# Performance work log

Hardware: AMD Instinct MI355X
Metric: run time of the kernel (lower is better)

## Reference

```python
import jax, jax.numpy as jnp
import numpy as np

N, C, H, W = 16, 512, 32, 32
NH = 8            # num_heads
HD = C // NH      # head dim c = 64
G = C // 4        # GroupNorm groups = 128
EPS = 1e-5


def conv1x1(X, Wt, b):
    # 1x1 Conv2d == per-pixel linear over channels
    return jnp.einsum('oc,nchw->nohw', Wt, X) + b[None, :, None, None]


def setup_inputs() -> dict:
    key = jax.random.key(0)
    ks = jax.random.split(key, 9)
    s = 0.02
    inp = {
        'X': jax.random.normal(ks[0], (N, C, H, W), jnp.float32),
        'Wq': jax.random.normal(ks[1], (C, C), jnp.float32) * s,
        'bq': jax.random.normal(ks[2], (C,), jnp.float32) * s,
        'Wk': jax.random.normal(ks[3], (C, C), jnp.float32) * s,
        'bk': jax.random.normal(ks[4], (C,), jnp.float32) * s,
        'Wv': jax.random.normal(ks[5], (C, C), jnp.float32) * s,
        'bv': jax.random.normal(ks[6], (C,), jnp.float32) * s,
        'Wo': jax.random.normal(ks[7], (C, C), jnp.float32) * s,
        'bo': jax.random.normal(ks[8], (C,), jnp.float32) * s,
        'gn_w': jnp.ones((C,), jnp.float32),
        'gn_b': jnp.zeros((C,), jnp.float32),
    }
    return inp


def reference(X, Wq, bq, Wk, bk, Wv, bv, Wo, bo, gn_w, gn_b):
    # NOTE: original torch code does  K, Q, V = (Q_conv(X), K_conv(X), V_conv(X))
    # i.e. K gets the Q_conv weights and Q gets the K_conv weights; mirror that.
    K = conv1x1(X, Wq, bq)
    Q = conv1x1(X, Wk, bk)
    V = conv1x1(X, Wv, bv)

    d = H * W
    Kh = K.reshape(N, NH, HD, d)  # [n,h,c,d]
    Qh = Q.reshape(N, NH, HD, d)
    Vh = V.reshape(N, NH, HD, d)

    # softmax-free channel attention: (Q^T K) then V (Q^T K)^T
    A = jnp.einsum('nhcd,nhcD->nhdD', Qh, Kh)   # [n,h,d,d]
    O = jnp.einsum('nhdD,nhcD->nhcd', A, Vh)    # [n,h,c,d]

    O = O.reshape(N, C, H, W)
    O = conv1x1(O, Wo, bo)

    # GroupNorm(G, C) with affine, eps=1e-5
    Og = O.reshape(N, G, C // G, H, W)
    mu = Og.mean(axis=(2, 3, 4), keepdims=True)
    var = Og.var(axis=(2, 3, 4), keepdims=True)
    On = ((Og - mu) * jax.lax.rsqrt(var + EPS)).reshape(N, C, H, W)
    On = On * gn_w[None, :, None, None] + gn_b[None, :, None, None]

    return On + X
```

## Files before the change

kernel.cpp:

```cpp
#include <hip/hip_runtime.h>
#include <hip/hip_bf16.h>

typedef __attribute__((ext_vector_type(8))) short s8v;
typedef __attribute__((ext_vector_type(4))) short s4v;
typedef __attribute__((ext_vector_type(4))) float f32x4;

#define MFMA_BF16 __builtin_amdgcn_mfma_f32_16x16x32_bf16

__device__ inline void gload_lds16(const __hip_bfloat16* g, __hip_bfloat16* l) {
  __builtin_amdgcn_global_load_lds(
      (const __attribute__((address_space(1))) void*)g,
      (__attribute__((address_space(3))) void*)l, 16, 0, 0);
}

__device__ inline short f2bs(float x) {
  __hip_bfloat16 b = __float2bfloat16(x);
  return *reinterpret_cast<short*>(&b);
}

__device__ inline void storeC(float* p, float v) { *p = v; }
__device__ inline void storeC(__hip_bfloat16* p, float v) { *p = __float2bfloat16(v); }

__global__ __launch_bounds__(256) void prep(const float* __restrict__ X,
                                            __hip_bfloat16* __restrict__ XT,
                                            __hip_bfloat16* __restrict__ Xc,
                                            const float* __restrict__ Wq,
                                            const float* __restrict__ Wv,
                                            const float* __restrict__ Wk,
                                            const float* __restrict__ Wo,
                                            const float* __restrict__ bq,
                                            const float* __restrict__ bv,
                                            __hip_bfloat16* __restrict__ WA,
                                            __hip_bfloat16* __restrict__ WkT,
                                            __hip_bfloat16* __restrict__ WOb,
                                            float* __restrict__ biasKV) {
  const int tid = threadIdx.x;
  if (blockIdx.z == 16) {
    const int blk = blockIdx.y * 16 + blockIdx.x;
#pragma unroll
    for (int t = 0; t < 8; ++t) {
      const int i = (blk * 8 + t) * 256 + tid;
      WA[i] = __float2bfloat16(Wq[i]);
      WA[262144 + i] = __float2bfloat16(Wv[i]);
      WOb[i] = __float2bfloat16(Wo[i]);
      WkT[i] = __float2bfloat16(Wk[(i & 511) * 512 + (i >> 9)]);
      if (i < 512) { biasKV[i] = bq[i]; biasKV[512 + i] = bv[i]; }
    }
    return;
  }
  __shared__ float tl[64][65];
  const int n = blockIdx.z;
  const int c0 = blockIdx.y * 64, p0 = blockIdx.x * 64;
  const int lr = tid >> 4, lc4 = (tid & 15) * 4;
  const float* Xp = X + ((long)n * 512 + c0) * 1024 + p0;
  __hip_bfloat16* Xcp = Xc + ((long)n * 512 + c0) * 1024 + p0;
#pragma unroll
  for (int i = 0; i < 4; ++i) {
    const int ch = i * 16 + lr;
    const float4 v = *(const float4*)&Xp[(long)ch * 1024 + lc4];
    tl[ch][lc4 + 0] = v.x; tl[ch][lc4 + 1] = v.y;
    tl[ch][lc4 + 2] = v.z; tl[ch][lc4 + 3] = v.w;
    s4v xo;
    xo[0] = f2bs(v.x); xo[1] = f2bs(v.y); xo[2] = f2bs(v.z); xo[3] = f2bs(v.w);
    *(s4v*)&Xcp[(long)ch * 1024 + lc4] = xo;
  }
  __syncthreads();
  __hip_bfloat16* XTp = XT + ((long)n * 1024 + p0) * 512 + c0;
#pragma unroll
  for (int i = 0; i < 4; ++i) {
    const int px = i * 16 + lr;
    s4v o;
#pragma unroll
    for (int e = 0; e < 4; ++e) o[e] = f2bs(tl[lc4 + e][px]);
    *(s4v*)&XTp[(long)px * 512 + lc4] = o;
  }
}

template <typename OutT, bool BROW>
__global__ __launch_bounds__(256) void gemm_nt(
    const __hip_bfloat16* __restrict__ A, long strideA,
    const __hip_bfloat16* __restrict__ B, long strideB,
    OutT* __restrict__ C, long strideC, int K, int ldc,
    const float* __restrict__ brow, long strideBrow) {
  A += blockIdx.z * strideA;
  B += blockIdx.z * strideB;
  C += blockIdx.z * strideC;
  const int m0 = blockIdx.y * 128;
  const int n0 = blockIdx.x * 128;
  const int tid = threadIdx.x;
  const int wid = tid >> 6, lane = tid & 63;
  const int wm = wid >> 1, wn = wid & 1;

  __shared__ __hip_bfloat16 As[128 * 64];
  __shared__ __hip_bfloat16 Bs[128 * 64];

  f32x4 acc[4][4] = {};

  const __hip_bfloat16* gA0 = A + (long)(m0 + wid * 32 + (lane >> 3)) * K + (lane & 7) * 8;
  const __hip_bfloat16* gB0 = B + (long)(n0 + wid * 32 + (lane >> 3)) * K + (lane & 7) * 8;

  for (int k0 = 0; k0 < K; k0 += 64) {
#pragma unroll
    for (int t = 0; t < 4; ++t) {
      gload_lds16(gA0 + (long)t * 8 * K + k0, &As[(wid * 32 + t * 8) * 64]);
      gload_lds16(gB0 + (long)t * 8 * K + k0, &Bs[(wid * 32 + t * 8) * 64]);
    }
    __syncthreads();
#pragma unroll
    for (int ks = 0; ks < 2; ++ks) {
      const int koff = ks * 32 + (lane >> 4) * 8;
      s8v a[4], b[4];
#pragma unroll
      for (int i = 0; i < 4; ++i)
        a[i] = *(const s8v*)&As[(wm * 64 + i * 16 + (lane & 15)) * 64 + koff];
#pragma unroll
      for (int j = 0; j < 4; ++j)
        b[j] = *(const s8v*)&Bs[(wn * 64 + j * 16 + (lane & 15)) * 64 + koff];
#pragma unroll
      for (int i = 0; i < 4; ++i)
#pragma unroll
        for (int j = 0; j < 4; ++j)
          acc[i][j] = MFMA_BF16(a[i], b[j], acc[i][j], 0, 0, 0);
    }
    __syncthreads();
  }

  const int cr = (lane >> 4) * 4;
  const int cc = lane & 15;
#pragma unroll
  for (int i = 0; i < 4; ++i) {
#pragma unroll
    for (int r = 0; r < 4; ++r) {
      const int gm = m0 + wm * 64 + i * 16 + cr + r;
      const float rb = BROW ? brow[blockIdx.z * strideBrow + gm] : 0.f;
#pragma unroll
      for (int j = 0; j < 4; ++j) {
        const int gn = n0 + wn * 64 + j * 16 + cc;
        storeC(&C[(long)gm * ldc + gn], acc[i][j][r] + rb);
      }
    }
  }
}

__global__ __launch_bounds__(512) void gemm_vkT(const __hip_bfloat16* __restrict__ V,
                                                const __hip_bfloat16* __restrict__ Kk,
                                                __hip_bfloat16* __restrict__ Mt) {
  const int n = blockIdx.x >> 3, h = blockIdx.x & 7;
  const int tid = threadIdx.x, wid = tid >> 6, lane = tid & 63;
  f32x4 acc[4][4] = {};
  const long colbase = (long)n * 1024 + wid * 128 + (lane >> 4) * 8;
  const __hip_bfloat16* Vb = V + (long)(h * 64 + (lane & 15)) * 16384 + colbase;
  const __hip_bfloat16* Kb = Kk + (long)(h * 64 + (lane & 15)) * 16384 + colbase;
#pragma unroll
  for (int kk = 0; kk < 128; kk += 32) {
    s8v a[4], b[4];
#pragma unroll
    for (int i = 0; i < 4; ++i) a[i] = *(const s8v*)(Vb + (long)i * 16 * 16384 + kk);
#pragma unroll
    for (int j = 0; j < 4; ++j) b[j] = *(const s8v*)(Kb + (long)j * 16 * 16384 + kk);
#pragma unroll
    for (int i = 0; i < 4; ++i)
#pragma unroll
      for (int j = 0; j < 4; ++j) acc[i][j] = MFMA_BF16(a[i], b[j], acc[i][j], 0, 0, 0);
  }
  __shared__ float part[4][4096];
  const int cr = (lane >> 4) * 4, cc = lane & 15;
  if (wid < 4) {
#pragma unroll
    for (int i = 0; i < 4; ++i)
#pragma unroll
      for (int r = 0; r < 4; ++r)
#pragma unroll
        for (int j = 0; j < 4; ++j)
          part[wid][(i * 16 + cr + r) * 64 + j * 16 + cc] = acc[i][j][r];
  }
  __syncthreads();
  if (wid >= 4) {
#pragma unroll
    for (int i = 0; i < 4; ++i)
#pragma unroll
      for (int r = 0; r < 4; ++r)
#pragma unroll
        for (int j = 0; j < 4; ++j)
          part[wid - 4][(i * 16 + cr + r) * 64 + j * 16 + cc] += acc[i][j][r];
  }
  __syncthreads();
  __hip_bfloat16* outp = Mt + ((long)n * 8 + h) * 4096;
  for (int e = tid; e < 4096; e += 512) {
    const float sum = part[0][e] + part[1][e] + part[2][e] + part[3][e];
    outp[(e & 63) * 64 + (e >> 6)] = __float2bfloat16(sum);
  }
}

__global__ __launch_bounds__(256) void wchain(const __hip_bfloat16* __restrict__ WOb,
                                              const __hip_bfloat16* __restrict__ WkT,
                                              const __hip_bfloat16* __restrict__ Mt,
                                              const float* __restrict__ bk,
                                              const float* __restrict__ bo,
                                              __hip_bfloat16* __restrict__ WPP,
                                              float* __restrict__ b2out) {
  const int c0 = blockIdx.x * 128, o0 = blockIdx.y * 128, n = blockIdx.z;
  const int tid = threadIdx.x, wid = tid >> 6, lane = tid & 63;
  const int wm = wid >> 1, wn = wid & 1;
  const int cr = (lane >> 4) * 4, cc = lane & 15;

  __shared__ __hip_bfloat16 WoS[128 * 64];
  __shared__ __hip_bfloat16 WkS[128 * 64];
  __shared__ __hip_bfloat16 MtS[64 * 64];
  __shared__ __hip_bfloat16 W1S[128 * 64];
  __shared__ float bkS[512];

  if (tid < 128) *(float4*)&bkS[tid * 4] = *(const float4*)&bk[tid * 4];

  f32x4 acc2[4][4] = {};
  float bacc = 0.f;
  const int r8 = lane >> 3, b8 = (lane & 7) * 8;

  for (int h = 0; h < 8; ++h) {
#pragma unroll
    for (int t = 0; t < 4; ++t) {
      const int row = wid * 32 + t * 8;
      gload_lds16(WOb + (long)(o0 + row + r8) * 512 + h * 64 + b8, &WoS[row * 64]);
      gload_lds16(WkT + (long)(c0 + row + r8) * 512 + h * 64 + b8, &WkS[row * 64]);
    }
    {
      const __hip_bfloat16* mg = Mt + ((long)n * 8 + h) * 4096;
      gload_lds16(mg + wid * 512 + lane * 8, &MtS[wid * 512]);
      gload_lds16(mg + 2048 + wid * 512 + lane * 8, &MtS[2048 + wid * 512]);
    }
    __syncthreads();

    f32x4 acc1[2][4] = {};
#pragma unroll
    for (int ks = 0; ks < 2; ++ks) {
      const int ko = ks * 32 + (lane >> 4) * 8;
      s8v aj[2], bw[4];
#pragma unroll
      for (int i = 0; i < 2; ++i)
        aj[i] = *(const s8v*)&MtS[(wn * 32 + i * 16 + cc) * 64 + ko];
#pragma unroll
      for (int t = 0; t < 4; ++t)
        bw[t] = *(const s8v*)&WoS[(wm * 64 + t * 16 + cc) * 64 + ko];
#pragma unroll
      for (int i = 0; i < 2; ++i)
#pragma unroll
        for (int t = 0; t < 4; ++t)
          acc1[i][t] = MFMA_BF16(aj[i], bw[t], acc1[i][t], 0, 0, 0);
    }
#pragma unroll
    for (int i = 0; i < 2; ++i)
#pragma unroll
      for (int t = 0; t < 4; ++t) {
        const int o = wm * 64 + t * 16 + cc;
        const int jb = wn * 32 + i * 16 + cr;
        s4v p;
#pragma unroll
        for (int r = 0; r < 4; ++r) p[r] = f2bs(acc1[i][t][r]);
        *(s4v*)((char*)W1S + ((o * 128 + jb * 2) ^ ((o & 7) << 4))) = p;
      }
    __syncthreads();

#pragma unroll
    for (int ks = 0; ks < 2; ++ks) {
      const int ko = ks * 32 + (lane >> 4) * 8;
      s8v a2[4], bw[4];
#pragma unroll
      for (int i = 0; i < 4; ++i) {
        const int o = wm * 64 + i * 16 + cc;
        a2[i] = *(const s8v*)((char*)W1S + ((o * 128 + ko * 2) ^ ((o & 7) << 4)));
      }
#pragma unroll
      for (int t = 0; t < 4; ++t)
        bw[t] = *(const s8v*)&WkS[(wn * 64 + t * 16 + cc) * 64 + ko];
#pragma unroll
      for (int i = 0; i < 4; ++i)
#pragma unroll
        for (int t = 0; t < 4; ++t)
          acc2[i][t] = MFMA_BF16(a2[i], bw[t], acc2[i][t], 0, 0, 0);
    }

    if (c0 == 0) {
      const int o = tid >> 1, half = tid & 1;
      float s = 0.f;
#pragma unroll
      for (int q = 0; q < 4; ++q) {
        const int jb = half * 64 + q * 16;
        const s8v w = *(const s8v*)((char*)W1S + ((o * 128 + jb) ^ ((o & 7) << 4)));
        const __hip_bfloat16* wb = (const __hip_bfloat16*)&w;
#pragma unroll
        for (int e = 0; e < 8; ++e)
          s += __bfloat162float(wb[e]) * bkS[h * 64 + half * 32 + q * 8 + e];
      }
      bacc += s;
    }
    __syncthreads();
  }

#pragma unroll
  for (int i = 0; i < 4; ++i)
#pragma unroll
    for (int r = 0; r < 4; ++r)
#pragma unroll
      for (int t = 0; t < 4; ++t)
        WPP[((long)n * 512 + o0 + wm * 64 + i * 16 + cr + r) * 512 +
            c0 + wn * 64 + t * 16 + cc] = __float2bfloat16(acc2[i][t][r]);
  if (c0 == 0) {
    const float tot = bacc + __shfl_xor(bacc, 1);
    if ((tid & 1) == 0) {
      const int o = tid >> 1;
      b2out[n * 512 + o0 + o] = tot + bo[o0 + o];
    }
  }
}

__global__ __launch_bounds__(256) void gn_res(const __hip_bfloat16* __restrict__ Y,
                                              const __hip_bfloat16* __restrict__ Xc,
                                              const float* __restrict__ gw,
                                              const float* __restrict__ gb,
                                              float* __restrict__ out) {
  const int n = blockIdx.x >> 7, g = blockIdx.x & 127;
  const long base = ((long)n * 512 + g * 4) * 1024;
  const int tid = threadIdx.x;
  float v[16];
  float s = 0.f, s2 = 0.f;
#pragma unroll
  for (int i = 0; i < 2; ++i) {
    const s8v x = *(const s8v*)&Y[base + ((long)(i * 256 + tid)) * 8];
#pragma unroll
    for (int e = 0; e < 8; ++e) {
      const float f = __bfloat162float(((const __hip_bfloat16*)&x)[e]);
      v[i * 8 + e] = f;
      s += f;
      s2 += f * f;
    }
  }
#pragma unroll
  for (int off = 32; off; off >>= 1) {
    s += __shfl_down(s, off);
    s2 += __shfl_down(s2, off);
  }
  __shared__ float rs[8];
  const int wid = tid >> 6, lane = tid & 63;
  if (lane == 0) { rs[wid] = s; rs[4 + wid] = s2; }
  __syncthreads();
  if (tid == 0) {
    const float ts = rs[0] + rs[1] + rs[2] + rs[3];
    const float t2 = rs[4] + rs[5] + rs[6] + rs[7];
    const float mu = ts * (1.f / 4096.f);
    const float var = t2 * (1.f / 4096.f) - mu * mu;
    rs[0] = mu;
    rs[1] = rsqrtf(var + 1e-5f);
  }
  __syncthreads();
  const float mu = rs[0], rstd = rs[1];
#pragma unroll
  for (int i = 0; i < 2; ++i) {
    const int chunk = i * 256 + tid;
    const long e0 = base + (long)chunk * 8;
    const int c = g * 4 + (chunk >> 7);
    const float sc = rstd * gw[c], sh = gb[c];
    const s8v xv = *(const s8v*)&Xc[e0];
    const __hip_bfloat16* xb = (const __hip_bfloat16*)&xv;
    float4 o0, o1;
    o0.x = (v[i * 8 + 0] - mu) * sc + sh + __bfloat162float(xb[0]);
    o0.y = (v[i * 8 + 1] - mu) * sc + sh + __bfloat162float(xb[1]);
    o0.z = (v[i * 8 + 2] - mu) * sc + sh + __bfloat162float(xb[2]);
    o0.w = (v[i * 8 + 3] - mu) * sc + sh + __bfloat162float(xb[3]);
    o1.x = (v[i * 8 + 4] - mu) * sc + sh + __bfloat162float(xb[4]);
    o1.y = (v[i * 8 + 5] - mu) * sc + sh + __bfloat162float(xb[5]);
    o1.z = (v[i * 8 + 6] - mu) * sc + sh + __bfloat162float(xb[6]);
    o1.w = (v[i * 8 + 7] - mu) * sc + sh + __bfloat162float(xb[7]);
    *(float4*)&out[e0] = o0;
    *(float4*)&out[e0 + 4] = o1;
  }
}

extern "C" void kernel_launch(void* const* d_in, const int* in_sizes, int n_in,
                              void* d_out, int out_size, void* d_ws, size_t ws_size,
                              hipStream_t stream) {
  const float* X  = (const float*)d_in[0];
  const float* Wq = (const float*)d_in[1];
  const float* bq = (const float*)d_in[2];
  const float* Wk = (const float*)d_in[3];
  const float* bk = (const float*)d_in[4];
  const float* Wv = (const float*)d_in[5];
  const float* bv = (const float*)d_in[6];
  const float* Wo = (const float*)d_in[7];
  const float* bo = (const float*)d_in[8];
  const float* gw = (const float*)d_in[9];
  const float* gb = (const float*)d_in[10];
  float* out = (float*)d_out;

  char* ws = (char*)d_ws;
  __hip_bfloat16* XT  = (__hip_bfloat16*)(ws + 0);
  __hip_bfloat16* KV  = (__hip_bfloat16*)(ws + 16777216);
  __hip_bfloat16* Y   = (__hip_bfloat16*)(ws + 16777216);
  __hip_bfloat16* WPP = (__hip_bfloat16*)(ws + 58720256);
  __hip_bfloat16* Mt  = (__hip_bfloat16*)(ws + 67108864);
  __hip_bfloat16* WA  = (__hip_bfloat16*)(ws + 68157440);
  __hip_bfloat16* WkT = (__hip_bfloat16*)(ws + 69206016);
  __hip_bfloat16* WOb = (__hip_bfloat16*)(ws + 69730304);
  float*          bKV = (float*)(ws + 70254592);
  float*          b2  = (float*)(ws + 70258688);
  __hip_bfloat16* Xc  = (__hip_bfloat16*)(ws + 75497472);

  prep<<<dim3(16, 8, 17), 256, 0, stream>>>(X, XT, Xc, Wq, Wv, Wk, Wo, bq, bv,
                                            WA, WkT, WOb, bKV);
  gemm_nt<__hip_bfloat16, true><<<dim3(128, 8, 1), 256, 0, stream>>>(
      WA, 0, XT, 0, KV, 0, 512, 16384, bKV, 0);
  gemm_vkT<<<128, 512, 0, stream>>>(KV + (long)512 * 16384, KV, Mt);
  wchain<<<dim3(4, 4, 16), 256, 0, stream>>>(WOb, WkT, Mt, bk, bo, WPP, b2);
  gemm_nt<__hip_bfloat16, true><<<dim3(8, 4, 16), 256, 0, stream>>>(
      WPP, 262144, XT, 524288, Y, 524288, 512, 1024, b2, 512);
  gn_res<<<2048, 256, 0, stream>>>(Y, Xc, gw, gb, out);
}
```

Baseline: 117.1 us.

## Double-buffer wchain LDS tiles to prefetch the next head during compute

Doubles the Wo, Wk and Mt shared-memory tiles in the wchain kernel so the loads for head h+1 are issued while head h is being computed. The plain __syncthreads calls are replaced with explicit waitcnt plus s_barrier pairs, and the barrier at the end of each iteration is dropped. The aim is to hide global-to-LDS load latency behind the two MFMA stages. In exchange, LDS use per block grows substantially, which can lower occupancy, and correctness now depends on the hand-placed waits.

```diff
diff --git a/kernel.cpp b/kernel.cpp
--- a/kernel.cpp
+++ b/kernel.cpp
@@ -204,31 +204,38 @@
   const int wm = wid >> 1, wn = wid & 1;
   const int cr = (lane >> 4) * 4, cc = lane & 15;
 
-  __shared__ __hip_bfloat16 WoS[128 * 64];
-  __shared__ __hip_bfloat16 WkS[128 * 64];
-  __shared__ __hip_bfloat16 MtS[64 * 64];
+  __shared__ __hip_bfloat16 WoS[2][128 * 64];
+  __shared__ __hip_bfloat16 WkS[2][128 * 64];
+  __shared__ __hip_bfloat16 MtS[2][64 * 64];
   __shared__ __hip_bfloat16 W1S[128 * 64];
   __shared__ float bkS[512];
 
   if (tid < 128) *(float4*)&bkS[tid * 4] = *(const float4*)&bk[tid * 4];
 
+  const int r8 = lane >> 3, b8 = (lane & 7) * 8;
+  auto STAGE = [&](int h, int buf) {
+#pragma unroll
+    for (int t = 0; t < 4; ++t) {
+      const int row = wid * 32 + t * 8;
+      gload_lds16(WOb + (long)(o0 + row + r8) * 512 + h * 64 + b8, &WoS[buf][row * 64]);
+      gload_lds16(WkT + (long)(c0 + row + r8) * 512 + h * 64 + b8, &WkS[buf][row * 64]);
+    }
+    const __hip_bfloat16* mg = Mt + ((long)n * 8 + h) * 4096;
+    gload_lds16(mg + wid * 512 + lane * 8, &MtS[buf][wid * 512]);
+    gload_lds16(mg + 2048 + wid * 512 + lane * 8, &MtS[buf][2048 + wid * 512]);
+  };
+
   f32x4 acc2[4][4] = {};
   float bacc = 0.f;
-  const int r8 = lane >> 3, b8 = (lane & 7) * 8;
+
+  STAGE(0, 0);
 
   for (int h = 0; h < 8; ++h) {
-#pragma unroll
-    for (int t = 0; t < 4; ++t) {
-      const int row = wid * 32 + t * 8;
-      gload_lds16(WOb + (long)(o0 + row + r8) * 512 + h * 64 + b8, &WoS[row * 64]);
-      gload_lds16(WkT + (long)(c0 + row + r8) * 512 + h * 64 + b8, &WkS[row * 64]);
-    }
-    {
-      const __hip_bfloat16* mg = Mt + ((long)n * 8 + h) * 4096;
-      gload_lds16(mg + wid * 512 + lane * 8, &MtS[wid * 512]);
-      gload_lds16(mg + 2048 + wid * 512 + lane * 8, &MtS[2048 + wid * 512]);
-    }
-    __syncthreads();
+    const int cur = h & 1;
+    asm volatile("s_waitcnt vmcnt(0)" ::: "memory");
+    __builtin_amdgcn_s_barrier();
+    __builtin_amdgcn_sched_barrier(0);
+    if (h < 7) STAGE(h + 1, cur ^ 1);
 
     f32x4 acc1[2][4] = {};
 #pragma unroll
@@ -237,10 +244,10 @@
       s8v aj[2], bw[4];
 #pragma unroll
       for (int i = 0; i < 2; ++i)
-        aj[i] = *(const s8v*)&MtS[(wn * 32 + i * 16 + cc) * 64 + ko];
+        aj[i] = *(const s8v*)&MtS[cur][(wn * 32 + i * 16 + cc) * 64 + ko];
 #pragma unroll
       for (int t = 0; t < 4; ++t)
-        bw[t] = *(const s8v*)&WoS[(wm * 64 + t * 16 + cc) * 64 + ko];
+        bw[t] = *(const s8v*)&WoS[cur][(wm * 64 + t * 16 + cc) * 64 + ko];
 #pragma unroll
       for (int i = 0; i < 2; ++i)
 #pragma unroll
@@ -258,7 +265,10 @@
         for (int r = 0; r < 4; ++r) p[r] = f2bs(acc1[i][t][r]);
         *(s4v*)((char*)W1S + ((o * 128 + jb * 2) ^ ((o & 7) << 4))) = p;
       }
-    __syncthreads();
+    asm volatile("s_waitcnt lgkmcnt(0)" ::: "memory");
+    __builtin_amdgcn_sched_barrier(0);
+    __builtin_amdgcn_s_barrier();
+    __builtin_amdgcn_sched_barrier(0);
 
 #pragma unroll
     for (int ks = 0; ks < 2; ++ks) {
@@ -271,7 +281,7 @@
       }
 #pragma unroll
       for (int t = 0; t < 4; ++t)
-        bw[t] = *(const s8v*)&WkS[(wn * 64 + t * 16 + cc) * 64 + ko];
+        bw[t] = *(const s8v*)&WkS[cur][(wn * 64 + t * 16 + cc) * 64 + ko];
 #pragma unroll
       for (int i = 0; i < 4; ++i)
 #pragma unroll
@@ -293,7 +303,6 @@
       }
       bacc += s;
     }
-    __syncthreads();
   }
 
 #pragma unroll
```

Result: no change. 118.5 us (+1.2%).

## Fuse final projection GEMM with GroupNorm and residual into one kernel

Applied to the files above, without the earlier changes.

Replaces the last per-batch GEMM (WPP×XT to Y) and the separate GroupNorm+residual kernel with one kernel. Each block computes 32 output channels across all 1024 pixels, keeps results in registers, reduces group statistics through shared memory, then writes the normalized output plus residual directly. This removes the bf16 Y round trip and one launch. In exchange the grid shrinks to 256 blocks, the inner loop is a simple load-sync-compute with no double buffering, and the output stores are narrow scalar writes.

```diff
diff --git a/kernel.cpp b/kernel.cpp
--- a/kernel.cpp
+++ b/kernel.cpp
@@ -313,65 +313,120 @@
   }
 }
 
-__global__ __launch_bounds__(256) void gn_res(const __hip_bfloat16* __restrict__ Y,
+__global__ __launch_bounds__(512, 4) void ygn(const __hip_bfloat16* __restrict__ WPP,
+                                              const __hip_bfloat16* __restrict__ XT,
+                                              const float* __restrict__ b2,
                                               const __hip_bfloat16* __restrict__ Xc,
                                               const float* __restrict__ gw,
                                               const float* __restrict__ gb,
                                               float* __restrict__ out) {
-  const int n = blockIdx.x >> 7, g = blockIdx.x & 127;
-  const long base = ((long)n * 512 + g * 4) * 1024;
-  const int tid = threadIdx.x;
-  float v[16];
-  float s = 0.f, s2 = 0.f;
-#pragma unroll
-  for (int i = 0; i < 2; ++i) {
-    const s8v x = *(const s8v*)&Y[base + ((long)(i * 256 + tid)) * 8];
-#pragma unroll
-    for (int e = 0; e < 8; ++e) {
-      const float f = __bfloat162float(((const __hip_bfloat16*)&x)[e]);
-      v[i * 8 + e] = f;
-      s += f;
-      s2 += f * f;
-    }
-  }
-#pragma unroll
-  for (int off = 32; off; off >>= 1) {
-    s += __shfl_down(s, off);
-    s2 += __shfl_down(s2, off);
-  }
-  __shared__ float rs[8];
-  const int wid = tid >> 6, lane = tid & 63;
-  if (lane == 0) { rs[wid] = s; rs[4 + wid] = s2; }
+  const int ch0 = blockIdx.x * 32, n = blockIdx.y;
+  const int tid = threadIdx.x, wid = tid >> 6, lane = tid & 63;
+  const int wm = wid & 1, wpx = wid >> 1;
+  const int cc = lane & 15, cr = (lane >> 4) * 4;
+
+  __shared__ __hip_bfloat16 As[32 * 512];
+  __shared__ __hip_bfloat16 Bs[256 * 64];
+  __shared__ float chS[32][2];
+  __shared__ float gS[8][2];
+
+  const __hip_bfloat16* wp = WPP + ((long)n * 512 + ch0) * 512;
+#pragma unroll
+  for (int t = 0; t < 4; ++t) {
+    const int row = wid * 4 + t;
+    gload_lds16(wp + (long)row * 512 + lane * 8, &As[row * 512]);
+  }
+  if (tid < 64) chS[tid >> 1][tid & 1] = 0.f;
+
+  const __hip_bfloat16* xb = XT + (long)n * 1024 * 512;
+  f32x4 acc[4][4] = {};
+
+#pragma unroll
+  for (int pc = 0; pc < 4; ++pc) {
+    for (int kc = 0; kc < 8; ++kc) {
+#pragma unroll
+      for (int t = 0; t < 4; ++t) {
+        const int r0 = wid * 32 + t * 8;
+        gload_lds16(xb + (long)(pc * 256 + r0 + (lane >> 3)) * 512 + kc * 64 + (lane & 7) * 8,
+                    &Bs[r0 * 64]);
+      }
+      __syncthreads();
+#pragma unroll
+      for (int ks = 0; ks < 2; ++ks) {
+        const int ko = ks * 32 + (lane >> 4) * 8;
+        const s8v a = *(const s8v*)&As[(wm * 16 + cc) * 512 + kc * 64 + ko];
+#pragma unroll
+        for (int j = 0; j < 4; ++j) {
+          const s8v b = *(const s8v*)&Bs[(wpx * 64 + j * 16 + cc) * 64 + ko];
+          acc[pc][j] = MFMA_BF16(a, b, acc[pc][j], 0, 0, 0);
+        }
+      }
+      __syncthreads();
+    }
+  }
+
+  float b2v[4], gwv[4], gbv[4];
+#pragma unroll
+  for (int r = 0; r < 4; ++r) {
+    const int ch = ch0 + wm * 16 + cr + r;
+    b2v[r] = b2[n * 512 + ch];
+    gwv[r] = gw[ch];
+    gbv[r] = gb[ch];
+  }
+  float s[4] = {}, s2[4] = {};
+#pragma unroll
+  for (int pc = 0; pc < 4; ++pc)
+#pragma unroll
+    for (int j = 0; j < 4; ++j)
+#pragma unroll
+      for (int r = 0; r < 4; ++r) {
+        const float v = acc[pc][j][r] + b2v[r];
+        acc[pc][j][r] = v;
+        s[r] += v;
+        s2[r] += v * v;
+      }
+#pragma unroll
+  for (int off = 1; off < 16; off <<= 1)
+#pragma unroll
+    for (int r = 0; r < 4; ++r) {
+      s[r] += __shfl_xor(s[r], off);
+      s2[r] += __shfl_xor(s2[r], off);
+    }
+  if (cc == 0) {
+#pragma unroll
+    for (int r = 0; r < 4; ++r) {
+      atomicAdd(&chS[wm * 16 + cr + r][0], s[r]);
+      atomicAdd(&chS[wm * 16 + cr + r][1], s2[r]);
+    }
+  }
   __syncthreads();
-  if (tid == 0) {
-    const float ts = rs[0] + rs[1] + rs[2] + rs[3];
-    const float t2 = rs[4] + rs[5] + rs[6] + rs[7];
+  if (tid < 8) {
+    const int g = tid;
+    float ts = 0.f, t2 = 0.f;
+#pragma unroll
+    for (int c = 0; c < 4; ++c) { ts += chS[g * 4 + c][0]; t2 += chS[g * 4 + c][1]; }
     const float mu = ts * (1.f / 4096.f);
     const float var = t2 * (1.f / 4096.f) - mu * mu;
-    rs[0] = mu;
-    rs[1] = rsqrtf(var + 1e-5f);
+    gS[g][0] = mu;
+    gS[g][1] = rsqrtf(var + 1e-5f);
   }
   __syncthreads();
-  const float mu = rs[0], rstd = rs[1];
-#pragma unroll
-  for (int i = 0; i < 2; ++i) {
-    const int chunk = i * 256 + tid;
-    const long e0 = base + (long)chunk * 8;
-    const int c = g * 4 + (chunk >> 7);
-    const float sc = rstd * gw[c], sh = gb[c];
-    const s8v xv = *(const s8v*)&Xc[e0];
-    const __hip_bfloat16* xb = (const __hip_bfloat16*)&xv;
-    float4 o0, o1;
-    o0.x = (v[i * 8 + 0] - mu) * sc + sh + __bfloat162float(xb[0]);
-    o0.y = (v[i * 8 + 1] - mu) * sc + sh + __bfloat162float(xb[1]);
-    o0.z = (v[i * 8 + 2] - mu) * sc + sh + __bfloat162float(xb[2]);
-    o0.w = (v[i * 8 + 3] - mu) * sc + sh + __bfloat162float(xb[3]);
-    o1.x = (v[i * 8 + 4] - mu) * sc + sh + __bfloat162float(xb[4]);
-    o1.y = (v[i * 8 + 5] - mu) * sc + sh + __bfloat162float(xb[5]);
-    o1.z = (v[i * 8 + 6] - mu) * sc + sh + __bfloat162float(xb[6]);
-    o1.w = (v[i * 8 + 7] - mu) * sc + sh + __bfloat162float(xb[7]);
-    *(float4*)&out[e0] = o0;
-    *(float4*)&out[e0 + 4] = o1;
+
+#pragma unroll
+  for (int r = 0; r < 4; ++r) {
+    const int chl = wm * 16 + cr + r;
+    const int ch = ch0 + chl;
+    const float mu = gS[chl >> 2][0], rstd = gS[chl >> 2][1];
+    const float sc = rstd * gwv[r], sh = gbv[r];
+    float* op = out + ((long)n * 512 + ch) * 1024;
+    const __hip_bfloat16* xr = Xc + ((long)n * 512 + ch) * 1024;
+#pragma unroll
+    for (int pc = 0; pc < 4; ++pc)
+#pragma unroll
+      for (int j = 0; j < 4; ++j) {
+        const int px = pc * 256 + wpx * 64 + j * 16 + cc;
+        op[px] = (acc[pc][j][r] - mu) * sc + sh + __bfloat162float(xr[px]);
+      }
   }
 }
 
@@ -394,7 +449,6 @@
   char* ws = (char*)d_ws;
   __hip_bfloat16* XT  = (__hip_bfloat16*)(ws + 0);
   __hip_bfloat16* KV  = (__hip_bfloat16*)(ws + 16777216);
-  __hip_bfloat16* Y   = (__hip_bfloat16*)(ws + 16777216);
   __hip_bfloat16* WPP = (__hip_bfloat16*)(ws + 58720256);
   __hip_bfloat16* Mt  = (__hip_bfloat16*)(ws + 67108864);
   __hip_bfloat16* WA  = (__hip_bfloat16*)(ws + 68157440);
@@ -410,7 +464,5 @@
       WA, 0, XT, 0, KV, 0, 512, 16384, bKV, 0);
   gemm_vkT<<<128, 512, 0, stream>>>(KV + (long)512 * 16384, KV, Mt);
   wchain<<<dim3(4, 4, 16), 256, 0, stream>>>(WOb, WkT, Mt, bk, bo, WPP, b2);
-  gemm_nt<__hip_bfloat16, true><<<dim3(8, 4, 16), 256, 0, stream>>>(
-      WPP, 262144, XT, 524288, Y, 524288, 512, 1024, b2, 512);
-  gn_res<<<2048, 256, 0, stream>>>(Y, Xc, gw, gb, out);
-}
+  ygn<<<dim3(16, 16), 512, 0, stream>>>(WPP, XT, b2, Xc, gw, gb, out);
+}
```

After: 137.7 us. 1.18x slower.
